# Kernel tuning notes

Measured on AMD Instinct MI355X. Metric: run time of the kernel, lower is better.

The kernel has to match this reference:

```python
import jax, jax.numpy as jnp
import numpy as np

B, A, N = 8, 256, 255
NB, NF, NG, NI = 128, 128, 25, 3
MAX_Z = 100
CUTOFF = 5.0
LOG2 = float(np.log(2.0))
EPS = 1e-12


def ssp(x):
    # shifted softplus: ln(0.5*e^x + 0.5)
    return jax.nn.softplus(x) - LOG2


def setup_inputs() -> dict:
    key = jax.random.key(0)
    ks = jax.random.split(key, 12)

    def w(k, shape, fan_in):
        b = 1.0 / np.sqrt(fan_in)
        return jax.random.uniform(k, shape, jnp.float32, -b, b)

    embedding = jax.random.normal(ks[0], (MAX_Z, NB), jnp.float32) * 0.1
    embedding = embedding.at[0].set(0.0)  # padding_idx=0

    inp = dict(
        atomic_numbers=jax.random.randint(ks[6], (B, A), 1, MAX_Z),
        positions=jax.random.normal(ks[7], (B, A, 3), jnp.float32) * 3.0,
        neighbors=jax.random.randint(ks[8], (B, A, N), 0, A),
        neighbor_mask=jnp.ones((B, A, N), jnp.float32),
        embedding=embedding,
        # filter-generating network (per interaction block)
        fw1=w(ks[1], (NI, NG, NF), NG), fb1=jnp.zeros((NI, NF), jnp.float32),
        fw2=w(ks[2], (NI, NF, NF), NF), fb2=jnp.zeros((NI, NF), jnp.float32),
        # cfconv in2f (no bias), f2out, and output dense
        in2f=w(ks[3], (NI, NB, NF), NB),
        f2out_w=w(ks[4], (NI, NF, NB), NF), f2out_b=jnp.zeros((NI, NB), jnp.float32),
        dense_w=w(ks[5], (NI, NB, NB), NB), dense_b=jnp.zeros((NI, NB), jnp.float32),
    )
    return inp


def _schnet_forward(atomic_numbers, positions, neighbors, neighbor_mask, embedding,
                    fw1, fb1, fw2, fb2, in2f, f2out_w, f2out_b, dense_w, dense_b):
    # atom embeddings [B, A, NB]
    x = embedding[atomic_numbers]

    gather = jax.vmap(lambda t, idx: t[idx])  # per-molecule gather along atom axis

    # AtomDistances: r_ij [B, A, N]
    nbr_pos = gather(positions, neighbors)            # [B, A, N, 3]
    dist_vec = nbr_pos - positions[:, :, None, :]
    r_ij = jnp.sqrt(jnp.sum(dist_vec * dist_vec, -1) + EPS)
    r_ij = r_ij * neighbor_mask                       # zero masked distances

    # GaussianSmearing: f_ij [B, A, N, NG]
    offsets = jnp.linspace(0.0, CUTOFF, NG, dtype=jnp.float32)
    width = offsets[1] - offsets[0]
    coeff = -0.5 / (width * width)
    f_ij = jnp.exp(coeff * (r_ij[..., None] - offsets) ** 2)

    # CosineCutoff [B, A, N]
    C = 0.5 * (jnp.cos(r_ij * (np.pi / CUTOFF)) + 1.0) * (r_ij < CUTOFF).astype(x.dtype)

    for i in range(NI):
        # filter network on expanded distances -> W [B, A, N, NF]
        W = ssp(jnp.einsum('bang,gf->banf', f_ij, fw1[i]) + fb1[i])
        W = jnp.einsum('banf,fg->bang', W, fw2[i]) + fb2[i]
        W = W * C[..., None]
        # cfconv: project, gather neighbors, filter, aggregate
        y = jnp.einsum('bad,df->baf', x, in2f[i])      # [B, A, NF]
        y_nbr = gather(y, neighbors)                   # [B, A, N, NF]
        agg = jnp.sum(y_nbr * W * neighbor_mask[..., None], axis=2)  # [B, A, NF]
        v = ssp(jnp.einsum('baf,fd->bad', agg, f2out_w[i]) + f2out_b[i])
        v = jnp.einsum('bad,de->bae', v, dense_w[i]) + dense_b[i]
        x = x + v
    return x


def reference(atomic_numbers, positions, neighbors, neighbor_mask, embedding,
              fw1, fb1, fw2, fb2, in2f, f2out_w, f2out_b, dense_w, dense_b):
    return _schnet_forward(atomic_numbers, positions, neighbors, neighbor_mask, embedding,
                           fw1, fb1, fw2, fb2, in2f, f2out_w, f2out_b, dense_w, dense_b)
```

## Files before the change

### kernel.cpp

```cpp
#include <hip/hip_runtime.h>


#define NATOM 2048
#define NNBR  255

typedef __attribute__((ext_vector_type(8))) short bf16x8;
typedef __attribute__((ext_vector_type(4))) float f32x4;

__device__ __forceinline__ unsigned short f2bf(float x){
  unsigned int u = __float_as_uint(x);
  u += 0x7fffu + ((u >> 16) & 1u);
  return (unsigned short)(u >> 16);
}

__device__ __forceinline__ float sspf(float x){
  return __logf(fmaf(0.5f, __expf(x), 0.5f));
}

__global__ void k_prep(const float* __restrict__ pos, const int* __restrict__ nbr,
                       const float* __restrict__ mask,
                       float* __restrict__ r_c, float* __restrict__ S_c,
                       int* __restrict__ nb_c, int* __restrict__ nact_g){
  __shared__ int wcnt[4];
  const int n = threadIdx.x;
  const int atom = (blockIdx.x & 7)*256 + (blockIdx.x >> 3);
  const int molBase = atom & ~255;
  const int wid = n >> 6, lane = n & 63;
  float r = 0.f, S = 0.f; int nb = 0;
  if (n < NNBR){
    nb = nbr[atom*NNBR + n];
    const float ax = pos[atom*3+0], ay = pos[atom*3+1], az = pos[atom*3+2];
    const int pi = (molBase + nb)*3;
    const float dx = pos[pi+0]-ax, dy = pos[pi+1]-ay, dz = pos[pi+2]-az;
    r = sqrtf(dx*dx + dy*dy + dz*dz + 1e-12f);
    const float m = mask[atom*NNBR + n];
    r *= m;
    const float C = (r < 5.0f) ? 0.5f*(__cosf(r*0.6283185307179586f)+1.0f) : 0.f;
    S = C * m;
  }
  r_c[atom*256 + n] = 0.f; S_c[atom*256 + n] = 0.f; nb_c[atom*256 + n] = 0;
  const unsigned long long b = __ballot(S != 0.f);
  const int rank = __popcll(b & ((1ull << lane) - 1ull));
  if (lane == 0) wcnt[wid] = __popcll(b);
  __syncthreads();
  int off = 0;
  for (int w = 0; w < 4; ++w) if (w < wid) off += wcnt[w];
  if (S != 0.f){
    const int slot = off + rank;
    r_c[atom*256 + slot] = r; S_c[atom*256 + slot] = S; nb_c[atom*256 + slot] = nb;
  }
  if (n == 0) nact_g[atom] = wcnt[0] + wcnt[1] + wcnt[2] + wcnt[3];
}

__global__ void k_prepw(const float* __restrict__ fw1, const float* __restrict__ fw2,
                        unsigned short* __restrict__ b1f, unsigned short* __restrict__ b2f){
  const int i = blockIdx.x / 10, part = blockIdx.x % 10, tid = threadIdx.x;
  if (part < 2){
    const int e = part*256 + tid;
    const float* w1 = fw1 + i*25*128;
    unsigned short* o1 = b1f + i*4096;
    const int n = e >> 6, l = e & 63, khi = l >> 4, llo = l & 15;
    unsigned short v[8];
    #pragma unroll
    for (int j = 0; j < 8; ++j){
      const int g = khi*8 + j;
      v[j] = f2bf((g < 25) ? w1[g*128 + n*16 + llo] : 0.f);
    }
    #pragma unroll
    for (int c = 0; c < 8; ++c)
      *(float4*)(o1 + c*12288 + e*8) = *(float4*)v;
  } else {
    const int e = (part - 2)*256 + tid;
    const float* w2 = fw2 + i*128*128;
    unsigned short* o2 = b2f + i*16384;
    const int frag = e >> 6, l = e & 63;
    const int k0 = frag >> 3, n = frag & 7, khi = l >> 4, llo = l & 15;
    unsigned short v[8];
    #pragma unroll
    for (int j = 0; j < 8; ++j){
      const int k = k0*32 + khi*8 + j;
      v[j] = f2bf(w2[k*128 + n*16 + llo]);
    }
    #pragma unroll
    for (int c = 0; c < 8; ++c)
      *(float4*)(o2 + c*49152 + e*8) = *(float4*)v;
  }
}

__global__ void k_init(const int* __restrict__ Z, const float* __restrict__ emb,
                       const float* __restrict__ in2f0,
                       float* __restrict__ x, float* __restrict__ y){
  __shared__ float xs[128];
  const int t = threadIdx.x;
  const int atom = (blockIdx.x & 7)*256 + (blockIdx.x >> 3);
  const float v = emb[Z[atom]*128 + t];
  x[atom*128 + t] = v; xs[t] = v;
  __syncthreads();
  float acc[8] = {0.f,0.f,0.f,0.f,0.f,0.f,0.f,0.f};
  #pragma unroll 4
  for (int d0 = 0; d0 < 128; d0 += 8)
    #pragma unroll
    for (int u = 0; u < 8; ++u)
      acc[u] = fmaf(xs[d0+u], in2f0[(d0+u)*128 + t], acc[u]);
  y[atom*128 + t] = ((acc[0]+acc[1])+(acc[2]+acc[3]))+((acc[4]+acc[5])+(acc[6]+acc[7]));
}

__global__ void k_mlp(const float* __restrict__ agg,
                      const float* __restrict__ f2w, const float* __restrict__ f2b,
                      const float* __restrict__ dw, const float* __restrict__ db,
                      const float* __restrict__ in2f_next,
                      float* __restrict__ x, float* __restrict__ y){
  __shared__ float aggL[128], v1[128], xs[128];
  const int t = threadIdx.x;
  const int atom = (blockIdx.x & 7)*256 + (blockIdx.x >> 3);
  aggL[t] = agg[atom*128 + t];
  __syncthreads();
  float a[8] = {0.f,0.f,0.f,0.f,0.f,0.f,0.f,0.f};
  #pragma unroll 4
  for (int d0 = 0; d0 < 128; d0 += 8)
    #pragma unroll
    for (int u = 0; u < 8; ++u)
      a[u] = fmaf(aggL[d0+u], f2w[(d0+u)*128 + t], a[u]);
  v1[t] = sspf(((a[0]+a[1])+(a[2]+a[3]))+((a[4]+a[5])+(a[6]+a[7])) + f2b[t]);
  __syncthreads();
  float b[8] = {0.f,0.f,0.f,0.f,0.f,0.f,0.f,0.f};
  #pragma unroll 4
  for (int d0 = 0; d0 < 128; d0 += 8)
    #pragma unroll
    for (int u = 0; u < 8; ++u)
      b[u] = fmaf(v1[d0+u], dw[(d0+u)*128 + t], b[u]);
  const float xn = x[atom*128 + t] +
      (((b[0]+b[1])+(b[2]+b[3]))+((b[4]+b[5])+(b[6]+b[7]))) + db[t];
  x[atom*128 + t] = xn;
  if (in2f_next){
    xs[t] = xn;
    __syncthreads();
    float yv[8] = {0.f,0.f,0.f,0.f,0.f,0.f,0.f,0.f};
    #pragma unroll 4
    for (int d0 = 0; d0 < 128; d0 += 8)
      #pragma unroll
      for (int u = 0; u < 8; ++u)
        yv[u] = fmaf(xs[d0+u], in2f_next[(d0+u)*128 + t], yv[u]);
    y[atom*128 + t] = ((yv[0]+yv[1])+(yv[2]+yv[3]))+((yv[4]+yv[5])+(yv[6]+yv[7]));
  }
}

__global__ __launch_bounds__(256, 2) void k_pairs(
    const float* __restrict__ r_c, const float* __restrict__ S_c,
    const int* __restrict__ nb_c, const int* __restrict__ nact_g,
    const float* __restrict__ y,
    const unsigned short* __restrict__ b1f_i, const unsigned short* __restrict__ b2f_i,
    const float* __restrict__ fb1, const float* __restrict__ fb2,
    float* __restrict__ agg){
  __shared__ __align__(16) char smem[49152];
  unsigned short* B2s = (unsigned short*)smem;

  const int tid = threadIdx.x;
  const int wid = tid >> 6, lane = tid & 63, lhi = lane >> 4, llo = lane & 15;
  const int sub = wid & 1, ai = wid >> 1;
  const int mol = blockIdx.x & 7;
  const int atom = mol*256 + (blockIdx.x >> 3)*2 + ai, molBase = mol*256;
  char* Hw = smem + 32768 + wid*4096;

  {
    const float4* src = (const float4*)(b2f_i + (size_t)mol*49152);
    float4* dst = (float4*)B2s;
    #pragma unroll
    for (int k = 0; k < 8; ++k) dst[k*256 + tid] = src[k*256 + tid];
  }
  bf16x8 B1[8];
  #pragma unroll
  for (int n = 0; n < 8; ++n)
    B1[n] = *(const bf16x8*)(b1f_i + (size_t)mol*12288 + (n*64 + lane)*8);
  float b1b[8], b2b[8];
  #pragma unroll
  for (int n = 0; n < 8; ++n){ b1b[n] = fb1[n*16 + llo]; b2b[n] = fb2[n*16 + llo]; }

  const int nact = nact_g[atom];
  const int ntiles = (nact + 15) >> 4;

  float aggp[8];
  #pragma unroll
  for (int n = 0; n < 8; ++n) aggp[n] = 0.f;

  const float STEP = 5.0f/24.0f;
  const float GC   = -11.52f;

  __syncthreads();

  for (int t = sub; t < ntiles; t += 2){
    const int row0 = t*16;
    const float r = r_c[atom*256 + row0 + llo];
    bf16x8 a1;
    #pragma unroll
    for (int jj = 0; jj < 8; ++jj){
      const int g = lhi*8 + jj;
      float v = 0.f;
      if (g < 25){ const float d = r - (float)g*STEP; v = __expf(GC*d*d); }
      a1[jj] = (short)f2bf(v);
    }
    f32x4 h[8];
    #pragma unroll
    for (int n = 0; n < 8; ++n){
      const f32x4 cin = {b1b[n], b1b[n], b1b[n], b1b[n]};
      h[n] = __builtin_amdgcn_mfma_f32_16x16x32_bf16(a1, B1[n], cin, 0, 0, 0);
    }
    #pragma unroll
    for (int n = 0; n < 8; ++n)
      #pragma unroll
      for (int j = 0; j < 4; ++j){
        const int lrow = 4*lhi + j;
        const float hv = sspf(h[n][j]);
        const int boff = (lrow*256 + (n*16 + llo)*2) ^ ((lrow & 7) << 4);
        *(unsigned short*)(Hw + boff) = f2bf(hv);
      }
    f32x4 acc[8];
    #pragma unroll
    for (int n = 0; n < 8; ++n) acc[n] = f32x4{b2b[n], b2b[n], b2b[n], b2b[n]};
    #pragma unroll
    for (int k0 = 0; k0 < 4; ++k0){
      const int boff = (llo*256 + k0*64 + lhi*16) ^ ((llo & 7) << 4);
      const bf16x8 a2 = *(const bf16x8*)(Hw + boff);
      #pragma unroll
      for (int n = 0; n < 8; ++n){
        const bf16x8 b2v = *(const bf16x8*)(B2s + ((k0*8 + n)*64 + lane)*8);
        acc[n] = __builtin_amdgcn_mfma_f32_16x16x32_bf16(a2, b2v, acc[n], 0, 0, 0);
      }
    }
    #pragma unroll
    for (int j = 0; j < 4; ++j){
      const int grow = row0 + 4*lhi + j;
      const float S = S_c[atom*256 + grow];
      const float* yrow = y + (molBase + nb_c[atom*256 + grow])*128;
      #pragma unroll
      for (int n = 0; n < 8; ++n)
        aggp[n] = fmaf(acc[n][j] * S, yrow[n*16 + llo], aggp[n]);
    }
  }

  #pragma unroll
  for (int n = 0; n < 8; ++n){
    aggp[n] += __shfl_xor(aggp[n], 16);
    aggp[n] += __shfl_xor(aggp[n], 32);
  }
  float* red = (float*)Hw;
  if (lane < 16){
    #pragma unroll
    for (int n = 0; n < 8; ++n) red[n*16 + lane] = aggp[n];
  }
  __syncthreads();
  if (sub == 0 && lane < 16){
    const float* red1 = (const float*)(smem + 32768 + (wid + 1)*4096);
    #pragma unroll
    for (int n = 0; n < 8; ++n)
      agg[atom*128 + n*16 + lane] = red[n*16 + lane] + red1[n*16 + lane];
  }
}

extern "C" void kernel_launch(void* const* d_in, const int* in_sizes, int n_in,
                              void* d_out, int out_size, void* d_ws, size_t ws_size,
                              hipStream_t stream){
  const int*   Z    = (const int*)  d_in[0];
  const float* pos  = (const float*)d_in[1];
  const int*   nbr  = (const int*)  d_in[2];
  const float* mask = (const float*)d_in[3];
  const float* emb  = (const float*)d_in[4];
  const float* fw1  = (const float*)d_in[5];
  const float* fb1  = (const float*)d_in[6];
  const float* fw2  = (const float*)d_in[7];
  const float* fb2  = (const float*)d_in[8];
  const float* in2f = (const float*)d_in[9];
  const float* f2w  = (const float*)d_in[10];
  const float* f2b  = (const float*)d_in[11];
  const float* dw   = (const float*)d_in[12];
  const float* db   = (const float*)d_in[13];
  float* x = (float*)d_out;

  char* ws = (char*)d_ws;
  float* y    = (float*)ws;
  float* agg  = (float*)(ws + 1*1024*1024);
  float* r_c  = (float*)(ws + 2*1024*1024);
  float* S_c  = (float*)(ws + 4*1024*1024);
  int*   nb_c = (int*)  (ws + 6*1024*1024);
  int*   nact = (int*)  (ws + 8*1024*1024);
  unsigned short* b1f = (unsigned short*)(ws + 8*1024*1024 + 16*1024);
  unsigned short* b2f = (unsigned short*)(ws + 8*1024*1024 + 256*1024);

  k_prepw<<<30,    256, 0, stream>>>(fw1, fw2, b1f, b2f);
  k_prep <<<NATOM, 256, 0, stream>>>(pos, nbr, mask, r_c, S_c, nb_c, nact);
  k_init <<<NATOM, 128, 0, stream>>>(Z, emb, in2f, x, y);
  for (int i = 0; i < 3; ++i){
    k_pairs<<<NATOM/2, 256, 0, stream>>>(r_c, S_c, nb_c, nact, y,
        b1f + i*4096, b2f + i*16384, fb1 + i*128, fb2 + i*128, agg);
    k_mlp  <<<NATOM, 128, 0, stream>>>(agg,
        f2w + i*16384, f2b + i*128, dw + i*16384, db + i*128,
        (i < 2) ? (in2f + (i+1)*16384) : nullptr, x, y);
  }
}
```

Baseline: 180.7 us.

## Read filter weights from global memory and assign one atom per block with four waves

The pair kernel no longer stages the second filter-layer weights in LDS. Each MFMA operand is now loaded straight from global (L1/L2-cached) memory, which shrinks shared memory from 48KB to 16KB and raises possible occupancy. Each block now processes one atom with four waves striding over neighbor tiles, instead of two atoms with two waves each, so the grid doubles. The neighbor index and scale loads are hoisted ahead of the MFMA chain to hide gather latency. The cost is repeated global loads of B2 operands inside the inner loop and more work per block to read weights and combine partial sums.

```diff
diff --git a/kernel.cpp b/kernel.cpp
--- a/kernel.cpp
+++ b/kernel.cpp
@@ -152,26 +152,18 @@
     const unsigned short* __restrict__ b1f_i, const unsigned short* __restrict__ b2f_i,
     const float* __restrict__ fb1, const float* __restrict__ fb2,
     float* __restrict__ agg){
-  __shared__ __align__(16) char smem[49152];
-  unsigned short* B2s = (unsigned short*)smem;
-
+  __shared__ __align__(16) char smem[16384];
   const int tid = threadIdx.x;
   const int wid = tid >> 6, lane = tid & 63, lhi = lane >> 4, llo = lane & 15;
-  const int sub = wid & 1, ai = wid >> 1;
   const int mol = blockIdx.x & 7;
-  const int atom = mol*256 + (blockIdx.x >> 3)*2 + ai, molBase = mol*256;
-  char* Hw = smem + 32768 + wid*4096;
-
-  {
-    const float4* src = (const float4*)(b2f_i + (size_t)mol*49152);
-    float4* dst = (float4*)B2s;
-    #pragma unroll
-    for (int k = 0; k < 8; ++k) dst[k*256 + tid] = src[k*256 + tid];
-  }
+  const int atom = mol*256 + (blockIdx.x >> 3), molBase = mol*256;
+  char* Hw = smem + wid*4096;
+
+  const unsigned short* b1p = b1f_i + (size_t)mol*12288;
+  const unsigned short* b2p = b2f_i + (size_t)mol*49152;
   bf16x8 B1[8];
   #pragma unroll
-  for (int n = 0; n < 8; ++n)
-    B1[n] = *(const bf16x8*)(b1f_i + (size_t)mol*12288 + (n*64 + lane)*8);
+  for (int n = 0; n < 8; ++n) B1[n] = *(const bf16x8*)(b1p + (n*64 + lane)*8);
   float b1b[8], b2b[8];
   #pragma unroll
   for (int n = 0; n < 8; ++n){ b1b[n] = fb1[n*16 + llo]; b2b[n] = fb2[n*16 + llo]; }
@@ -186,10 +178,15 @@
   const float STEP = 5.0f/24.0f;
   const float GC   = -11.52f;
 
-  __syncthreads();
-
-  for (int t = sub; t < ntiles; t += 2){
+  for (int t = wid; t < ntiles; t += 4){
     const int row0 = t*16;
+    float S4[4]; const float* yp[4];
+    #pragma unroll
+    for (int j = 0; j < 4; ++j){
+      const int grow = row0 + 4*lhi + j;
+      S4[j] = S_c[atom*256 + grow];
+      yp[j] = y + (molBase + nb_c[atom*256 + grow])*128 + llo;
+    }
     const float r = r_c[atom*256 + row0 + llo];
     bf16x8 a1;
     #pragma unroll
@@ -223,18 +220,16 @@
       const bf16x8 a2 = *(const bf16x8*)(Hw + boff);
       #pragma unroll
       for (int n = 0; n < 8; ++n){
-        const bf16x8 b2v = *(const bf16x8*)(B2s + ((k0*8 + n)*64 + lane)*8);
+        const bf16x8 b2v = *(const bf16x8*)(b2p + ((k0*8 + n)*64 + lane)*8);
         acc[n] = __builtin_amdgcn_mfma_f32_16x16x32_bf16(a2, b2v, acc[n], 0, 0, 0);
       }
     }
     #pragma unroll
     for (int j = 0; j < 4; ++j){
-      const int grow = row0 + 4*lhi + j;
-      const float S = S_c[atom*256 + grow];
-      const float* yrow = y + (molBase + nb_c[atom*256 + grow])*128;
+      const float S = S4[j];
       #pragma unroll
       for (int n = 0; n < 8; ++n)
-        aggp[n] = fmaf(acc[n][j] * S, yrow[n*16 + llo], aggp[n]);
+        aggp[n] = fmaf(acc[n][j] * S, yp[j][n*16], aggp[n]);
     }
   }
 
@@ -249,11 +244,15 @@
     for (int n = 0; n < 8; ++n) red[n*16 + lane] = aggp[n];
   }
   __syncthreads();
-  if (sub == 0 && lane < 16){
-    const float* red1 = (const float*)(smem + 32768 + (wid + 1)*4096);
-    #pragma unroll
-    for (int n = 0; n < 8; ++n)
-      agg[atom*128 + n*16 + lane] = red[n*16 + lane] + red1[n*16 + lane];
+  if (wid == 0 && lane < 16){
+    #pragma unroll
+    for (int n = 0; n < 8; ++n){
+      float s = 0.f;
+      #pragma unroll
+      for (int k = 0; k < 4; ++k)
+        s += ((const float*)(smem + k*4096))[n*16 + lane];
+      agg[atom*128 + n*16 + lane] = s;
+    }
   }
 }
 
@@ -290,7 +289,7 @@
   k_prep <<<NATOM, 256, 0, stream>>>(pos, nbr, mask, r_c, S_c, nb_c, nact);
   k_init <<<NATOM, 128, 0, stream>>>(Z, emb, in2f, x, y);
   for (int i = 0; i < 3; ++i){
-    k_pairs<<<NATOM/2, 256, 0, stream>>>(r_c, S_c, nb_c, nact, y,
+    k_pairs<<<NATOM, 256, 0, stream>>>(r_c, S_c, nb_c, nact, y,
         b1f + i*4096, b2f + i*16384, fb1 + i*128, fb2 + i*128, agg);
     k_mlp  <<<NATOM, 128, 0, stream>>>(agg,
         f2w + i*16384, f2b + i*128, dw + i*16384, db + i*128,
```

Result: slower. 366.4 us (+102.8%).

## Keep filter hidden layer in registers via transposed MFMA and fold bias

Applied to the files above, without the earlier changes.

The first filter GEMM is computed transposed (B1 as A operand), so its output fragment lands directly in the layout the second GEMM needs as its A operand. This removes the per-tile LDS write/read round trip of the hidden activations. The second GEMM switches to the 16x16x16 bf16 MFMA, with the fw2 weights re-laid-out in prep to match. The fb1 bias is folded into the first GEMM as an extra constant-1 Gaussian column, and the S and neighbor-index loads are hoisted to the top of each tile. It trades LDS traffic and the sync-free write/read for twice as many, smaller MFMA instructions, and it lowers the LDS footprint.

```diff
diff --git a/kernel.cpp b/kernel.cpp
--- a/kernel.cpp
+++ b/kernel.cpp
@@ -5,7 +5,14 @@
 #define NNBR  255
 
 typedef __attribute__((ext_vector_type(8))) short bf16x8;
+typedef __attribute__((ext_vector_type(4))) short bf16x4;
 typedef __attribute__((ext_vector_type(4))) float f32x4;
+
+#if defined(__HIP_DEVICE_COMPILE__)
+#define MFMA16(A,B,C) __builtin_amdgcn_mfma_f32_16x16x16bf16_1k(A,B,C,0,0,0)
+#else
+#define MFMA16(A,B,C) (C)
+#endif
 
 __device__ __forceinline__ unsigned short f2bf(float x){
   unsigned int u = __float_as_uint(x);
@@ -52,19 +59,24 @@
   if (n == 0) nact_g[atom] = wcnt[0] + wcnt[1] + wcnt[2] + wcnt[3];
 }
 
-__global__ void k_prepw(const float* __restrict__ fw1, const float* __restrict__ fw2,
+__global__ void k_prepw(const float* __restrict__ fw1, const float* __restrict__ fb1,
+                        const float* __restrict__ fw2,
                         unsigned short* __restrict__ b1f, unsigned short* __restrict__ b2f){
   const int i = blockIdx.x / 10, part = blockIdx.x % 10, tid = threadIdx.x;
   if (part < 2){
     const int e = part*256 + tid;
     const float* w1 = fw1 + i*25*128;
+    const float* b1 = fb1 + i*128;
     unsigned short* o1 = b1f + i*4096;
     const int n = e >> 6, l = e & 63, khi = l >> 4, llo = l & 15;
     unsigned short v[8];
     #pragma unroll
     for (int j = 0; j < 8; ++j){
       const int g = khi*8 + j;
-      v[j] = f2bf((g < 25) ? w1[g*128 + n*16 + llo] : 0.f);
+      float w = 0.f;
+      if (g < 25) w = w1[g*128 + n*16 + llo];
+      else if (g == 25) w = b1[n*16 + llo];
+      v[j] = f2bf(w);
     }
     #pragma unroll
     for (int c = 0; c < 8; ++c)
@@ -73,14 +85,14 @@
     const int e = (part - 2)*256 + tid;
     const float* w2 = fw2 + i*128*128;
     unsigned short* o2 = b2f + i*16384;
-    const int frag = e >> 6, l = e & 63;
-    const int k0 = frag >> 3, n = frag & 7, khi = l >> 4, llo = l & 15;
+    const int idx = e >> 6, l = e & 63;
+    const int s = idx >> 2, p = idx & 3, lhi = l >> 4, llo = l & 15;
     unsigned short v[8];
     #pragma unroll
-    for (int j = 0; j < 8; ++j){
-      const int k = k0*32 + khi*8 + j;
-      v[j] = f2bf(w2[k*128 + n*16 + llo]);
-    }
+    for (int h = 0; h < 2; ++h)
+      #pragma unroll
+      for (int jj = 0; jj < 4; ++jj)
+        v[h*4 + jj] = f2bf(w2[(s*16 + lhi*4 + jj)*128 + (2*p + h)*16 + llo]);
     #pragma unroll
     for (int c = 0; c < 8; ++c)
       *(float4*)(o2 + c*49152 + e*8) = *(float4*)v;
@@ -150,17 +162,17 @@
     const int* __restrict__ nb_c, const int* __restrict__ nact_g,
     const float* __restrict__ y,
     const unsigned short* __restrict__ b1f_i, const unsigned short* __restrict__ b2f_i,
-    const float* __restrict__ fb1, const float* __restrict__ fb2,
+    const float* __restrict__ fb2,
     float* __restrict__ agg){
-  __shared__ __align__(16) char smem[49152];
+  __shared__ __align__(16) char smem[34816];
   unsigned short* B2s = (unsigned short*)smem;
+  float* redA = (float*)(smem + 32768);
 
   const int tid = threadIdx.x;
   const int wid = tid >> 6, lane = tid & 63, lhi = lane >> 4, llo = lane & 15;
   const int sub = wid & 1, ai = wid >> 1;
   const int mol = blockIdx.x & 7;
   const int atom = mol*256 + (blockIdx.x >> 3)*2 + ai, molBase = mol*256;
-  char* Hw = smem + 32768 + wid*4096;
 
   {
     const float4* src = (const float4*)(b2f_i + (size_t)mol*49152);
@@ -168,13 +180,13 @@
     #pragma unroll
     for (int k = 0; k < 8; ++k) dst[k*256 + tid] = src[k*256 + tid];
   }
+  const unsigned short* b1p = b1f_i + (size_t)mol*12288;
   bf16x8 B1[8];
   #pragma unroll
-  for (int n = 0; n < 8; ++n)
-    B1[n] = *(const bf16x8*)(b1f_i + (size_t)mol*12288 + (n*64 + lane)*8);
-  float b1b[8], b2b[8];
+  for (int n = 0; n < 8; ++n) B1[n] = *(const bf16x8*)(b1p + (n*64 + lane)*8);
+  float b2b[8];
   #pragma unroll
-  for (int n = 0; n < 8; ++n){ b1b[n] = fb1[n*16 + llo]; b2b[n] = fb2[n*16 + llo]; }
+  for (int n = 0; n < 8; ++n) b2b[n] = fb2[n*16 + llo];
 
   const int nact = nact_g[atom];
   const int ntiles = (nact + 15) >> 4;
@@ -190,6 +202,13 @@
 
   for (int t = sub; t < ntiles; t += 2){
     const int row0 = t*16;
+    float S4[4]; int rb4[4];
+    #pragma unroll
+    for (int j = 0; j < 4; ++j){
+      const int grow = row0 + 4*lhi + j;
+      S4[j] = S_c[atom*256 + grow];
+      rb4[j] = (molBase + nb_c[atom*256 + grow])*128 + llo;
+    }
     const float r = r_c[atom*256 + row0 + llo];
     bf16x8 a1;
     #pragma unroll
@@ -197,44 +216,40 @@
       const int g = lhi*8 + jj;
       float v = 0.f;
       if (g < 25){ const float d = r - (float)g*STEP; v = __expf(GC*d*d); }
+      else if (g == 25) v = 1.0f;
       a1[jj] = (short)f2bf(v);
     }
     f32x4 h[8];
-    #pragma unroll
-    for (int n = 0; n < 8; ++n){
-      const f32x4 cin = {b1b[n], b1b[n], b1b[n], b1b[n]};
-      h[n] = __builtin_amdgcn_mfma_f32_16x16x32_bf16(a1, B1[n], cin, 0, 0, 0);
-    }
+    const f32x4 zero4 = {0.f,0.f,0.f,0.f};
     #pragma unroll
     for (int n = 0; n < 8; ++n)
-      #pragma unroll
-      for (int j = 0; j < 4; ++j){
-        const int lrow = 4*lhi + j;
-        const float hv = sspf(h[n][j]);
-        const int boff = (lrow*256 + (n*16 + llo)*2) ^ ((lrow & 7) << 4);
-        *(unsigned short*)(Hw + boff) = f2bf(hv);
+      h[n] = __builtin_amdgcn_mfma_f32_16x16x32_bf16(B1[n], a1, zero4, 0, 0, 0);
+    bf16x4 a2[8];
+    #pragma unroll
+    for (int n = 0; n < 8; ++n)
+      #pragma unroll
+      for (int j = 0; j < 4; ++j)
+        a2[n][j] = (short)f2bf(sspf(h[n][j]));
+    f32x4 acc[8];
+    #pragma unroll
+    for (int n = 0; n < 8; ++n) acc[n] = f32x4{b2b[n], b2b[n], b2b[n], b2b[n]};
+    #pragma unroll
+    for (int s = 0; s < 8; ++s)
+      #pragma unroll
+      for (int p = 0; p < 4; ++p){
+        const bf16x8 w = *(const bf16x8*)(B2s + ((s*4 + p)*64 + lane)*8);
+        const bf16x4 wlo = {w[0], w[1], w[2], w[3]};
+        const bf16x4 whi = {w[4], w[5], w[6], w[7]};
+        acc[2*p]   = MFMA16(a2[s], wlo, acc[2*p]);
+        acc[2*p+1] = MFMA16(a2[s], whi, acc[2*p+1]);
       }
-    f32x4 acc[8];
-    #pragma unroll
-    for (int n = 0; n < 8; ++n) acc[n] = f32x4{b2b[n], b2b[n], b2b[n], b2b[n]};
-    #pragma unroll
-    for (int k0 = 0; k0 < 4; ++k0){
-      const int boff = (llo*256 + k0*64 + lhi*16) ^ ((llo & 7) << 4);
-      const bf16x8 a2 = *(const bf16x8*)(Hw + boff);
-      #pragma unroll
-      for (int n = 0; n < 8; ++n){
-        const bf16x8 b2v = *(const bf16x8*)(B2s + ((k0*8 + n)*64 + lane)*8);
-        acc[n] = __builtin_amdgcn_mfma_f32_16x16x32_bf16(a2, b2v, acc[n], 0, 0, 0);
-      }
-    }
     #pragma unroll
     for (int j = 0; j < 4; ++j){
-      const int grow = row0 + 4*lhi + j;
-      const float S = S_c[atom*256 + grow];
-      const float* yrow = y + (molBase + nb_c[atom*256 + grow])*128;
+      const float S = S4[j];
+      const float* yrow = y + rb4[j];
       #pragma unroll
       for (int n = 0; n < 8; ++n)
-        aggp[n] = fmaf(acc[n][j] * S, yrow[n*16 + llo], aggp[n]);
+        aggp[n] = fmaf(acc[n][j] * S, yrow[n*16], aggp[n]);
     }
   }
 
@@ -243,14 +258,14 @@
     aggp[n] += __shfl_xor(aggp[n], 16);
     aggp[n] += __shfl_xor(aggp[n], 32);
   }
-  float* red = (float*)Hw;
+  float* red = redA + wid*128;
   if (lane < 16){
     #pragma unroll
     for (int n = 0; n < 8; ++n) red[n*16 + lane] = aggp[n];
   }
   __syncthreads();
   if (sub == 0 && lane < 16){
-    const float* red1 = (const float*)(smem + 32768 + (wid + 1)*4096);
+    const float* red1 = redA + (wid + 1)*128;
     #pragma unroll
     for (int n = 0; n < 8; ++n)
       agg[atom*128 + n*16 + lane] = red[n*16 + lane] + red1[n*16 + lane];
@@ -286,12 +301,12 @@
   unsigned short* b1f = (unsigned short*)(ws + 8*1024*1024 + 16*1024);
   unsigned short* b2f = (unsigned short*)(ws + 8*1024*1024 + 256*1024);
 
-  k_prepw<<<30,    256, 0, stream>>>(fw1, fw2, b1f, b2f);
+  k_prepw<<<30,    256, 0, stream>>>(fw1, fb1, fw2, b1f, b2f);
   k_prep <<<NATOM, 256, 0, stream>>>(pos, nbr, mask, r_c, S_c, nb_c, nact);
   k_init <<<NATOM, 128, 0, stream>>>(Z, emb, in2f, x, y);
   for (int i = 0; i < 3; ++i){
     k_pairs<<<NATOM/2, 256, 0, stream>>>(r_c, S_c, nb_c, nact, y,
-        b1f + i*4096, b2f + i*16384, fb1 + i*128, fb2 + i*128, agg);
+        b1f + i*4096, b2f + i*16384, fb2 + i*128, agg);
     k_mlp  <<<NATOM, 128, 0, stream>>>(agg,
         f2w + i*16384, f2b + i*128, dw + i*16384, db + i*128,
         (i < 2) ? (in2f + (i+1)*16384) : nullptr, x, y);
```

After: 213.5 us. 18.2% more time.
